# Performance work log

Hardware: AMD Instinct MI355X
Metric: run time of the kernel (lower is better)

## Reference

```python
import jax, jax.numpy as jnp
import numpy as np

N, E, D, H, C = 40000, 640000, 128, 4, 32  # nodes, edges, in_hid, heads, out_channels/head
NUM_NODE_TYPE, NUM_EDGE_TYPE = 8, 8
NEG_SLOPE = 0.2
EDGE_TYPE_SELF = 0


def setup_inputs() -> dict:
    key = jax.random.key(0)
    ks = jax.random.split(key, 12)
    x = jax.random.normal(ks[0], (N, D), dtype=jnp.float32)
    # build edges with no self-loops (the module filters src==dst before adding self-loops)
    src = jax.random.randint(ks[1], (E,), 0, N, dtype=jnp.int32)
    off = jax.random.randint(ks[2], (E,), 1, N, dtype=jnp.int32)
    dst = (src + off) % N
    edge_index = jnp.stack([src, dst])  # [2, E]
    node_type = jax.random.randint(ks[3], (N,), 0, NUM_NODE_TYPE, dtype=jnp.int32)
    edge_type = jax.random.randint(ks[4], (E,), 0, NUM_EDGE_TYPE, dtype=jnp.int32)
    g = 0.05
    Wq = jax.random.normal(ks[5], (H * C, D), dtype=jnp.float32) * g
    Wk = jax.random.normal(ks[6], (H * C, D), dtype=jnp.float32) * g
    Wv = jax.random.normal(ks[7], (H * C, D), dtype=jnp.float32) * g
    att_i = jax.random.normal(ks[8], (1, H, C), dtype=jnp.float32) * g
    att_j = jax.random.normal(ks[9], (1, H, C), dtype=jnp.float32) * g
    bias = jnp.zeros((H * C,), dtype=jnp.float32)
    node_emb_table = jax.random.normal(ks[10], (NUM_NODE_TYPE, D), dtype=jnp.float32) * g
    edge_emb_table = jax.random.normal(ks[11], (NUM_EDGE_TYPE, D), dtype=jnp.float32) * g
    return {"x": x, "edge_index": edge_index, "node_type": node_type,
            "edge_type": edge_type, "Wq": Wq, "Wk": Wk, "Wv": Wv,
            "att_i": att_i, "att_j": att_j, "bias": bias,
            "node_emb_table": node_emb_table, "edge_emb_table": edge_emb_table}


def reference(x, edge_index, node_type, edge_type, Wq, Wk, Wv,
              att_i, att_j, bias, node_emb_table, edge_emb_table):
    n = x.shape[0]
    # node-type embedding add
    x = x + node_emb_table[node_type]                       # [N, D]
    xq = x @ Wq.T                                           # [N, H*C]
    # add self-loops (input edges contain no src==dst by construction)
    self_idx = jnp.arange(n, dtype=edge_index.dtype)
    src = jnp.concatenate([edge_index[0], self_idx])        # [E+N]
    dst = jnp.concatenate([edge_index[1], self_idx])        # [E+N]
    et = jnp.concatenate([edge_type,
                          jnp.full((n,), EDGE_TYPE_SELF, dtype=edge_type.dtype)])
    edge_emb = edge_emb_table[et]                           # [E+N, D]
    # message: per-edge gather + K/V linear + additive attention
    x_j = x[src] + edge_emb                                 # [E+N, D]
    xq_i = xq[dst].reshape(-1, H, C)                        # [E+N, H, C]
    x_k = (x_j @ Wk.T).reshape(-1, H, C)
    x_v = (x_j @ Wv.T).reshape(-1, H, C)
    alpha = (xq_i * att_i).sum(-1) + (x_k * att_j).sum(-1)  # [E+N, H]
    alpha = jax.nn.leaky_relu(alpha, NEG_SLOPE)
    # segment softmax over destination nodes (PyG softmax, eps=1e-16)
    amax = jax.ops.segment_max(alpha, dst, num_segments=n)  # [N, H]
    alpha = jnp.exp(alpha - amax[dst])
    denom = jax.ops.segment_sum(alpha, dst, num_segments=n)
    alpha = alpha / (denom[dst] + 1e-16)
    # scatter-add weighted values
    out = jax.ops.segment_sum(x_v * alpha[..., None], dst, num_segments=n)  # [N, H, C]
    return out.reshape(n, H * C) + bias
```

## Files before the change

### kernel.cpp

```cpp
#include <hip/hip_runtime.h>
#include <math.h>

#define NN 40000
#define NE 640000
#define D 128
#define NH 4
#define NC 32
#define NEG 0.2f
#define SXB 782

typedef __attribute__((ext_vector_type(8))) short bf16x8;
typedef __attribute__((ext_vector_type(4))) float f32x4;

__device__ __forceinline__ unsigned pack_bf16(float a, float b) {
  unsigned ua = __float_as_uint(a), ub = __float_as_uint(b);
  ua = (ua + 0x7FFFu + ((ua >> 16) & 1u)) >> 16;
  ub = (ub + 0x7FFFu + ((ub >> 16) & 1u)) & 0xFFFF0000u;
  return ub | ua;
}

__device__ __forceinline__ bf16x8 to_bf16x8(float4 a, float4 b) {
  union { bf16x8 v; unsigned u[4]; } r;
  r.u[0] = pack_bf16(a.x, a.y);
  r.u[1] = pack_bf16(a.z, a.w);
  r.u[2] = pack_bf16(b.x, b.y);
  r.u[3] = pack_bf16(b.z, b.w);
  return r.v;
}

__device__ __forceinline__ float4 f4add(float4 a, float4 b) {
  return make_float4(a.x + b.x, a.y + b.y, a.z + b.z, a.w + b.w);
}

__global__ __launch_bounds__(256) void k_tables(
    const float* __restrict__ Wq, const float* __restrict__ Wk,
    const float* __restrict__ Wv,
    const float* __restrict__ att_i, const float* __restrict__ att_j,
    const float* __restrict__ eemb,
    float* __restrict__ ev, float* __restrict__ a_et,
    unsigned* __restrict__ Wvh, int* __restrict__ counts) {
  __shared__ float sm[1024];
  int b = blockIdx.x, t = threadIdx.x;
  if (b == 0) {
    for (int j = t; j < 1024; j += 256) {
      int isq = (j < 512);
      int h = (j >> 7) & 3, d = j & 127;
      const float* __restrict__ Wm = isq ? Wq : Wk;
      const float* __restrict__ am = isq ? att_i : att_j;
      float s = 0.f;
#pragma unroll
      for (int c = 0; c < NC; ++c) s = fmaf(am[h * NC + c], Wm[(h * NC + c) * D + d], s);
      sm[j] = s;
    }
    __syncthreads();
    for (int j = t; j < 1024; j += 256) {
      int r = j >> 6;
      int c2 = (j & 63) * 2;
      float a = 0.f, bb = 0.f;
      if (r < 8) { a = sm[r * 128 + c2]; bb = sm[r * 128 + c2 + 1]; }
      Wvh[(128 + r) * 64 + (j & 63)] = pack_bf16(a, bb);
    }
    if (t < 32) {
      int ty = t >> 2, hh = t & 3;
      const float* wrow = sm + 512 + hh * 128;
      const float* __restrict__ emb = eemb + ty * D;
      float s = 0.f;
#pragma unroll 8
      for (int d = 0; d < D; ++d) s = fmaf(wrow[d], emb[d], s);
      a_et[t] = s;
    }
  } else if (b <= 8) {
    int ty = b - 1;
    if (t < 128) sm[t] = eemb[ty * D + t];
    __syncthreads();
    if (t < 128) {
      const float4* __restrict__ wr = (const float4*)(Wv + (size_t)t * D);
      const float4* __restrict__ er = (const float4*)sm;
      float s = 0.f;
#pragma unroll
      for (int k = 0; k < 32; ++k) {
        float4 ww = wr[k], ee = er[k];
        s = fmaf(ww.x, ee.x, s); s = fmaf(ww.y, ee.y, s);
        s = fmaf(ww.z, ee.z, s); s = fmaf(ww.w, ee.w, s);
      }
      ev[ty * D + t] = s;
    }
  } else if (b <= 16) {
    int j0 = (b - 9) * 1024;
    for (int j = j0 + t; j < j0 + 1024; j += 256)
      Wvh[j] = pack_bf16(Wv[2 * j], Wv[2 * j + 1]);
  } else {
    int i = (b - 17) * 256 + t;
    if (i < NN / 4) ((int4*)counts)[i] = make_int4(0, 0, 0, 0);
  }
}

__global__ __launch_bounds__(256) void k_sx(
    const int* __restrict__ ei, const int* __restrict__ etype,
    int* __restrict__ counts, unsigned* __restrict__ packed,
    const float* __restrict__ x, const int* __restrict__ node_type,
    const float* __restrict__ nemb, const unsigned* __restrict__ Wvh,
    unsigned* __restrict__ xvh, float* __restrict__ aq, float* __restrict__ ak) {
  int t = threadIdx.x;
  if (blockIdx.x < SXB) {
    int i = blockIdx.x * 256 + t;
    if (i < NE / 4) {
      int4 s4 = ((const int4*)ei)[i];
      int4 d4 = ((const int4*)(ei + NE))[i];
      int4 t4 = ((const int4*)etype)[i];
      int r;
      r = atomicAdd(&counts[d4.x], 1);
      if (r < 64) packed[(d4.x << 6) + r] = (unsigned)s4.x | ((unsigned)t4.x << 16);
      r = atomicAdd(&counts[d4.y], 1);
      if (r < 64) packed[(d4.y << 6) + r] = (unsigned)s4.y | ((unsigned)t4.y << 16);
      r = atomicAdd(&counts[d4.z], 1);
      if (r < 64) packed[(d4.z << 6) + r] = (unsigned)s4.z | ((unsigned)t4.z << 16);
      r = atomicAdd(&counts[d4.w], 1);
      if (r < 64) packed[(d4.w << 6) + r] = (unsigned)s4.w | ((unsigned)t4.w << 16);
    } else if (i < NE / 4 + NN) {
      int n = i - NE / 4;
      int r = atomicAdd(&counts[n], 1);
      if (r < 64) packed[(n << 6) + r] = (unsigned)n;
    }
    return;
  }
  int bb = blockIdx.x - SXB;
  int w = t >> 6, l = t & 63;
  int quad = l >> 4, col = l & 15;
  int n0w = bb * 64 + w * 16;
  int node = n0w + col;
  int ntA = node_type[node];
  const float4* __restrict__ xr = (const float4*)(x + (size_t)node * D);
  const float4* __restrict__ nr = (const float4*)(nemb + (size_t)ntA * D);
  bf16x8 afr[4];
#pragma unroll
  for (int s = 0; s < 4; ++s) {
    const float4* p = xr + s * 8 + quad * 2;
    const float4* q4 = nr + s * 8 + quad * 2;
    afr[s] = to_bf16x8(f4add(p[0], q4[0]), f4add(p[1], q4[1]));
  }
  f32x4 acc[9];
#pragma unroll
  for (int ct = 0; ct < 9; ++ct) acc[ct] = (f32x4){0.f, 0.f, 0.f, 0.f};
#pragma unroll
  for (int ct = 0; ct < 9; ++ct) {
    const unsigned* __restrict__ brow = Wvh + (size_t)(ct * 16 + col) * 64;
#pragma unroll
    for (int s = 0; s < 4; ++s) {
      bf16x8 bfr = *(const bf16x8*)(brow + s * 16 + quad * 4);
      acc[ct] = __builtin_amdgcn_mfma_f32_16x16x32_bf16(afr[s], bfr, acc[ct], 0, 0, 0);
    }
  }
  int nodes[4];
#pragma unroll
  for (int r = 0; r < 4; ++r) nodes[r] = n0w + quad * 4 + r;
#pragma unroll
  for (int ct = 0; ct < 8; ++ct) {
#pragma unroll
    for (int r = 0; r < 4; ++r) {
      float val = acc[ct][r];
      float pv = __shfl_xor(val, 1);
      if (!(col & 1)) {
        xvh[nodes[r] * 64 + ct * 8 + (col >> 1)] = pack_bf16(val, pv);
      }
    }
  }
  if (col < 4) {
#pragma unroll
    for (int r = 0; r < 4; ++r) aq[nodes[r] * NH + col] = acc[8][r];
  } else if (col < 8) {
#pragma unroll
    for (int r = 0; r < 4; ++r) ak[nodes[r] * NH + (col - 4)] = acc[8][r];
  }
}

__global__ __launch_bounds__(256) void k_gather(const int* __restrict__ counts,
        const unsigned* __restrict__ packed,
        const float* __restrict__ aq, const float* __restrict__ ak,
        const float* __restrict__ a_et, const unsigned* __restrict__ xvh,
        const float* __restrict__ ev, const float* __restrict__ bias,
        float* __restrict__ out) {
  int n = (int)((blockIdx.x * blockDim.x + threadIdx.x) >> 6);
  int l = threadIdx.x & 63;
  if (n >= NN) return;
  int g = l >> 3, q = l & 7;
  int h = q >> 1;
  float aqh = aq[n * NH + h];
  int e0 = n << 6;
  int deg = min(counts[n], 64);
  int e1 = e0 + deg;
  const uint4* __restrict__ xv4 = (const uint4*)xvh;
  float acc[16];
#pragma unroll
  for (int k = 0; k < 16; ++k) acc[k] = 0.f;
  float ps[8];
#pragma unroll
  for (int k = 0; k < 8; ++k) ps[k] = 0.f;
  int iters = (deg + 7) >> 3;
  int e = e0 + g;
  bool val = (e < e1);
  unsigned rec = packed[val ? e : e0];
  int src = (int)(rec & 0xFFFFu), etc = (int)(rec >> 16);
  float sA = ak[src * NH + h] + a_et[etc * NH + h];
  uint4 vb0 = xv4[src * 16 + 2 * q];
  uint4 vb1 = xv4[src * 16 + 2 * q + 1];
  for (int it = 0; it < iters; ++it) {
    int e2 = e + 8;
    bool v2 = (e2 < e1);
    float sAn = 0.f; int etn = 0;
    uint4 vb0n = make_uint4(0, 0, 0, 0), vb1n = make_uint4(0, 0, 0, 0);
    if (it + 1 < iters) {
      unsigned rec2 = packed[v2 ? e2 : e0];
      int s2 = (int)(rec2 & 0xFFFFu);
      etn = (int)(rec2 >> 16);
      sAn = ak[s2 * NH + h] + a_et[etn * NH + h];
      vb0n = xv4[s2 * 16 + 2 * q];
      vb1n = xv4[s2 * 16 + 2 * q + 1];
    }
    float s = aqh + sA;
    s = (s > 0.f) ? s : NEG * s;
    float p = val ? __expf(s) : 0.f;
#pragma unroll
    for (int tt = 0; tt < 8; ++tt) ps[tt] += (etc == tt) ? p : 0.f;
    float f[16];
    f[0]  = __uint_as_float(vb0.x << 16); f[1]  = __uint_as_float(vb0.x & 0xFFFF0000u);
    f[2]  = __uint_as_float(vb0.y << 16); f[3]  = __uint_as_float(vb0.y & 0xFFFF0000u);
    f[4]  = __uint_as_float(vb0.z << 16); f[5]  = __uint_as_float(vb0.z & 0xFFFF0000u);
    f[6]  = __uint_as_float(vb0.w << 16); f[7]  = __uint_as_float(vb0.w & 0xFFFF0000u);
    f[8]  = __uint_as_float(vb1.x << 16); f[9]  = __uint_as_float(vb1.x & 0xFFFF0000u);
    f[10] = __uint_as_float(vb1.y << 16); f[11] = __uint_as_float(vb1.y & 0xFFFF0000u);
    f[12] = __uint_as_float(vb1.z << 16); f[13] = __uint_as_float(vb1.z & 0xFFFF0000u);
    f[14] = __uint_as_float(vb1.w << 16); f[15] = __uint_as_float(vb1.w & 0xFFFF0000u);
#pragma unroll
    for (int k = 0; k < 16; ++k) acc[k] = fmaf(p, f[k], acc[k]);
    e = e2; val = v2; sA = sAn; etc = etn; vb0 = vb0n; vb1 = vb1n;
  }
#pragma unroll
  for (int tt = 0; tt < 8; ++tt) {
    ps[tt] += __shfl_xor(ps[tt], 8);
    ps[tt] += __shfl_xor(ps[tt], 16);
    ps[tt] += __shfl_xor(ps[tt], 32);
  }
  float dsum = ((ps[0] + ps[1]) + (ps[2] + ps[3])) + ((ps[4] + ps[5]) + (ps[6] + ps[7]));
  float psg = ps[0];
#pragma unroll
  for (int tt = 1; tt < 8; ++tt) psg = (g == tt) ? ps[tt] : psg;
  const float4* __restrict__ ep = (const float4*)(ev + g * D + 16 * q);
  float4 ea0 = ep[0], ea1 = ep[1], ea2 = ep[2], ea3 = ep[3];
  acc[0]  = fmaf(psg, ea0.x, acc[0]);
  acc[1]  = fmaf(psg, ea0.y, acc[1]);
  acc[2]  = fmaf(psg, ea0.z, acc[2]);
  acc[3]  = fmaf(psg, ea0.w, acc[3]);
  acc[4]  = fmaf(psg, ea1.x, acc[4]);
  acc[5]  = fmaf(psg, ea1.y, acc[5]);
  acc[6]  = fmaf(psg, ea1.z, acc[6]);
  acc[7]  = fmaf(psg, ea1.w, acc[7]);
  acc[8]  = fmaf(psg, ea2.x, acc[8]);
  acc[9]  = fmaf(psg, ea2.y, acc[9]);
  acc[10] = fmaf(psg, ea2.z, acc[10]);
  acc[11] = fmaf(psg, ea2.w, acc[11]);
  acc[12] = fmaf(psg, ea3.x, acc[12]);
  acc[13] = fmaf(psg, ea3.y, acc[13]);
  acc[14] = fmaf(psg, ea3.z, acc[14]);
  acc[15] = fmaf(psg, ea3.w, acc[15]);
#pragma unroll
  for (int k = 0; k < 16; ++k) {
    acc[k] += __shfl_xor(acc[k], 8);
    acc[k] += __shfl_xor(acc[k], 16);
    acc[k] += __shfl_xor(acc[k], 32);
  }
  if (g == 0) {
    float inv = 1.f / (dsum + 1e-16f);
    const float4* __restrict__ b4 = (const float4*)(bias + 16 * q);
    float4* __restrict__ op = (float4*)(out + (size_t)n * D + 16 * q);
#pragma unroll
    for (int k4 = 0; k4 < 4; ++k4) {
      float4 bb = b4[k4];
      op[k4] = make_float4(acc[4 * k4 + 0] * inv + bb.x,
                           acc[4 * k4 + 1] * inv + bb.y,
                           acc[4 * k4 + 2] * inv + bb.z,
                           acc[4 * k4 + 3] * inv + bb.w);
    }
  }
}

extern "C" void kernel_launch(void* const* d_in, const int* in_sizes, int n_in,
                              void* d_out, int out_size, void* d_ws, size_t ws_size,
                              hipStream_t stream) {
  const float* x      = (const float*)d_in[0];
  const int*   ei     = (const int*)d_in[1];
  const int*   ntype  = (const int*)d_in[2];
  const int*   etype  = (const int*)d_in[3];
  const float* Wq     = (const float*)d_in[4];
  const float* Wk     = (const float*)d_in[5];
  const float* Wv     = (const float*)d_in[6];
  const float* att_i  = (const float*)d_in[7];
  const float* att_j  = (const float*)d_in[8];
  const float* bias   = (const float*)d_in[9];
  const float* nemb   = (const float*)d_in[10];
  const float* eemb   = (const float*)d_in[11];
  float* out = (float*)d_out;

  float* ws     = (float*)d_ws;
  unsigned* xvh = (unsigned*)ws;
  float* aq     = ws + (size_t)NN * 64;
  float* ak     = aq + NN * NH;
  float* ev     = ak + NN * NH;
  float* a_et   = ev + 1024;
  unsigned* Wvh = (unsigned*)(a_et + 32);
  int*   counts = (int*)(Wvh + 9216);
  unsigned* packed = (unsigned*)(counts + NN);

  k_tables<<<dim3(64), dim3(256), 0, stream>>>(Wq, Wk, Wv, att_i, att_j, eemb,
                                               ev, a_et, Wvh, counts);
  k_sx<<<dim3(SXB + 625), dim3(256), 0, stream>>>(ei, etype, counts, packed,
                                                  x, ntype, nemb, Wvh, xvh, aq, ak);
  k_gather<<<dim3((NN + 3) / 4), dim3(256), 0, stream>>>(counts, packed, aq, ak, a_et,
                                                         xvh, ev, bias, out);
}
```

Measured before the change: 192.8 us.

## Interleave edge scatter blocks with node GEMM blocks and synthesize self-loops in gather

The fused kernel's scatter blocks now handle one edge per thread and are interleaved 4:1 with the node-projection GEMM blocks, instead of a leading group of scatter blocks followed by GEMM blocks. The aim is to overlap the atomic-heavy edge bucketing with compute-bound work across the GPU and to spread atomic contention. Self-loop edges are no longer written into the buckets: the gather kernel synthesizes the self edge as an extra slot, which removes NN atomics and stores. The bucket cap drops to 63 real edges plus the implicit self-loop. The trade-off is more blocks, per-thread scalar loads instead of int4 loads, and an extra branch in the gather.

```diff
diff --git a/kernel.cpp b/kernel.cpp
--- a/kernel.cpp
+++ b/kernel.cpp
@@ -7,7 +7,6 @@
 #define NH 4
 #define NC 32
 #define NEG 0.2f
-#define SXB 782
 
 typedef __attribute__((ext_vector_type(8))) short bf16x8;
 typedef __attribute__((ext_vector_type(4))) float f32x4;
@@ -95,36 +94,24 @@
   }
 }
 
-__global__ __launch_bounds__(256) void k_sx(
+__global__ __launch_bounds__(256) void k_sxi(
     const int* __restrict__ ei, const int* __restrict__ etype,
     int* __restrict__ counts, unsigned* __restrict__ packed,
     const float* __restrict__ x, const int* __restrict__ node_type,
     const float* __restrict__ nemb, const unsigned* __restrict__ Wvh,
     unsigned* __restrict__ xvh, float* __restrict__ aq, float* __restrict__ ak) {
-  int t = threadIdx.x;
-  if (blockIdx.x < SXB) {
-    int i = blockIdx.x * 256 + t;
-    if (i < NE / 4) {
-      int4 s4 = ((const int4*)ei)[i];
-      int4 d4 = ((const int4*)(ei + NE))[i];
-      int4 t4 = ((const int4*)etype)[i];
-      int r;
-      r = atomicAdd(&counts[d4.x], 1);
-      if (r < 64) packed[(d4.x << 6) + r] = (unsigned)s4.x | ((unsigned)t4.x << 16);
-      r = atomicAdd(&counts[d4.y], 1);
-      if (r < 64) packed[(d4.y << 6) + r] = (unsigned)s4.y | ((unsigned)t4.y << 16);
-      r = atomicAdd(&counts[d4.z], 1);
-      if (r < 64) packed[(d4.z << 6) + r] = (unsigned)s4.z | ((unsigned)t4.z << 16);
-      r = atomicAdd(&counts[d4.w], 1);
-      if (r < 64) packed[(d4.w << 6) + r] = (unsigned)s4.w | ((unsigned)t4.w << 16);
-    } else if (i < NE / 4 + NN) {
-      int n = i - NE / 4;
-      int r = atomicAdd(&counts[n], 1);
-      if (r < 64) packed[(n << 6) + r] = (unsigned)n;
-    }
+  int b = blockIdx.x, t = threadIdx.x;
+  if (b % 5 != 0) {
+    int sb = b - (b + 4) / 5;
+    int i = sb * 256 + t;
+    int src = ei[i];
+    int dst = ei[NE + i];
+    int et  = etype[i];
+    int r = atomicAdd(&counts[dst], 1);
+    if (r < 63) packed[(dst << 6) + r] = (unsigned)src | ((unsigned)et << 16);
     return;
   }
-  int bb = blockIdx.x - SXB;
+  int bb = b / 5;
   int w = t >> 6, l = t & 63;
   int quad = l >> 4, col = l & 15;
   int n0w = bb * 64 + w * 16;
@@ -187,8 +174,8 @@
   int h = q >> 1;
   float aqh = aq[n * NH + h];
   int e0 = n << 6;
-  int deg = min(counts[n], 64);
-  int e1 = e0 + deg;
+  int deg = min(counts[n], 63);
+  int m = deg + 1;
   const uint4* __restrict__ xv4 = (const uint4*)xvh;
   float acc[16];
 #pragma unroll
@@ -196,21 +183,21 @@
   float ps[8];
 #pragma unroll
   for (int k = 0; k < 8; ++k) ps[k] = 0.f;
-  int iters = (deg + 7) >> 3;
-  int e = e0 + g;
-  bool val = (e < e1);
-  unsigned rec = packed[val ? e : e0];
+  int iters = (m + 7) >> 3;
+  int i = g;
+  bool val = (i < m);
+  unsigned rec = (val && i < deg) ? packed[e0 + i] : (unsigned)n;
   int src = (int)(rec & 0xFFFFu), etc = (int)(rec >> 16);
   float sA = ak[src * NH + h] + a_et[etc * NH + h];
   uint4 vb0 = xv4[src * 16 + 2 * q];
   uint4 vb1 = xv4[src * 16 + 2 * q + 1];
   for (int it = 0; it < iters; ++it) {
-    int e2 = e + 8;
-    bool v2 = (e2 < e1);
+    int i2 = i + 8;
+    bool v2 = (i2 < m);
     float sAn = 0.f; int etn = 0;
     uint4 vb0n = make_uint4(0, 0, 0, 0), vb1n = make_uint4(0, 0, 0, 0);
     if (it + 1 < iters) {
-      unsigned rec2 = packed[v2 ? e2 : e0];
+      unsigned rec2 = (v2 && i2 < deg) ? packed[e0 + i2] : (unsigned)n;
       int s2 = (int)(rec2 & 0xFFFFu);
       etn = (int)(rec2 >> 16);
       sAn = ak[s2 * NH + h] + a_et[etn * NH + h];
@@ -233,7 +220,7 @@
     f[14] = __uint_as_float(vb1.w << 16); f[15] = __uint_as_float(vb1.w & 0xFFFF0000u);
 #pragma unroll
     for (int k = 0; k < 16; ++k) acc[k] = fmaf(p, f[k], acc[k]);
-    e = e2; val = v2; sA = sAn; etc = etn; vb0 = vb0n; vb1 = vb1n;
+    i = i2; val = v2; sA = sAn; etc = etn; vb0 = vb0n; vb1 = vb1n;
   }
 #pragma unroll
   for (int tt = 0; tt < 8; ++tt) {
@@ -313,8 +300,8 @@
 
   k_tables<<<dim3(64), dim3(256), 0, stream>>>(Wq, Wk, Wv, att_i, att_j, eemb,
                                                ev, a_et, Wvh, counts);
-  k_sx<<<dim3(SXB + 625), dim3(256), 0, stream>>>(ei, etype, counts, packed,
-                                                  x, ntype, nemb, Wvh, xvh, aq, ak);
+  k_sxi<<<dim3(3125), dim3(256), 0, stream>>>(ei, etype, counts, packed,
+                                              x, ntype, nemb, Wvh, xvh, aq, ak);
   k_gather<<<dim3((NN + 3) / 4), dim3(256), 0, stream>>>(counts, packed, aq, ak, a_et,
                                                          xvh, ev, bias, out);
 }
```

Result: faster. 175.8 us (-8.8%).
